# Kernel optimization log

Hardware: AMD Instinct MI355X
Metric: run time of the kernel (lower is better)

Reference implementation:

```python
import jax, jax.numpy as jnp
import numpy as np

B, NP, NC, E, C = 4, 512, 256, 128, 32
NBUCKET = 20


def soft_one_hot_linspace(x, start=0.0, end=15.0, number=NBUCKET):
    # e3nn soft_one_hot_linspace, basis='smooth_finite', cutoff=True
    values = jnp.linspace(start, end, number + 2)[1:-1]
    step = (end - start) / (number + 1)
    diff = (x[..., None] - values) / step

    def sus(y):  # exp(-1/y) for y>0 else 0 (smooth unit step)
        return jnp.where(y > 0.0, jnp.exp(-1.0 / jnp.where(y > 0.0, y, 1.0)), 0.0)

    return 1.14136 * jnp.exp(2.0) * sus(diff + 1.0) * sus(1.0 - diff)


def _init_linear(k, fan_in, fan_out):
    k1, k2 = jax.random.split(k)
    bound = 1.0 / np.sqrt(fan_in)
    W = jax.random.uniform(k1, (fan_in, fan_out), jnp.float32, -bound, bound)
    b = jax.random.uniform(k2, (fan_out,), jnp.float32, -bound, bound)
    return W, b


def setup_inputs() -> dict:
    key = jax.random.key(0)
    ks = jax.random.split(key, 12)
    inp = {}
    inp["z"] = jax.random.normal(ks[0], (B, NP, NC, E), jnp.float32)
    inp["z_mask"] = jax.random.randint(ks[1], (B, NP, NC), 0, 2) == 1
    inp["pocket_rep"] = jax.random.normal(ks[2], (B, NP, E), jnp.float32)
    inp["candidate_dis"] = jax.random.uniform(ks[3], (B, NP, NC), jnp.float32) * 16.0
    inp["W_lin"], inp["b_lin"] = _init_linear(ks[4], E, C)
    inp["W_dis"], inp["b_dis"] = _init_linear(ks[5], NBUCKET, C)
    inp["W_energy"], inp["b_energy"] = _init_linear(ks[6], C, 1)
    inp["W_gate"], inp["b_gate"] = _init_linear(ks[7], C, 1)
    inp["bias"] = jnp.ones((1,), jnp.float32)
    inp["W_energy_p"], inp["b_energy_p"] = _init_linear(ks[8], C, 1)
    inp["W_gate_p"], inp["b_gate_p"] = _init_linear(ks[9], C, 1)
    inp["bias_p"] = jnp.ones((1,), jnp.float32)
    inp["W_out"], inp["b_out"] = _init_linear(ks[10], E * C, E)
    return inp


def reference(z, z_mask, pocket_rep, candidate_dis,
              W_lin, b_lin, W_dis, b_dis,
              W_energy, b_energy, W_gate, b_gate, bias,
              W_energy_p, b_energy_p, W_gate_p, b_gate_p, bias_p,
              W_out, b_out):
    b, n_p, n_c, e = z.shape
    c = W_lin.shape[1]
    # linear + transpose(3,1): [B,Np,Nc,E] -> [B,C,Nc,Np]
    zc = jnp.transpose(z @ W_lin + b_lin, (0, 3, 2, 1))
    # softmax over last dim (Np)
    zc = jax.nn.softmax(zc, axis=-1)
    # distance-bucket bias: [B,Np,Nc,20] -> [B,Np,Nc,C] -> view [B,C,Nc,Np]
    edge_emb = soft_one_hot_linspace(candidate_dis)
    dis_bias = (edge_emb @ W_dis + b_dis).reshape(b, c, n_c, n_p)
    zc = zc + dis_bias
    # z_mask.repeat(C,1,1).view(B,C,Nc,Np) -- literal torch element order
    mask_rep = jnp.tile(z_mask, (c, 1, 1)).reshape(b, c, n_c, n_p)
    zc = jnp.where(mask_rep, jnp.asarray(1e-09, zc.dtype), zc)
    # gated energy heads on z.transpose(3,1): [B,Np,Nc,C]
    zt = jnp.transpose(zc, (0, 3, 2, 1))
    zm = z_mask.astype(zc.dtype)
    pair_energy = (jax.nn.sigmoid(zt @ W_gate + b_gate) * (zt @ W_energy + b_energy))[..., 0] * zm
    affinity_pred = jax.nn.leaky_relu(bias + pair_energy.sum(axis=(-1, -2)))
    pair_energy_p = (jax.nn.sigmoid(zt @ W_gate_p + b_gate_p) * (zt @ W_energy_p + b_energy_p))[..., 0] * zm
    prmsd_pred = jax.nn.leaky_relu(bias_p + pair_energy_p.sum(axis=(-1, -2)))
    # ligand rep: bmm([B,C*Nc,Np], [B,Np,E]) -> [B,Nc,C*E] -> Linear
    lig = jnp.einsum('bcln,bne->bcle', zc, pocket_rep)  # [B,C,Nc,E]
    lig = jnp.transpose(lig, (0, 2, 1, 3)).reshape(b, n_c, c * e)
    ligand_rep = lig @ W_out + b_out
    return (ligand_rep, affinity_pred, prmsd_pred)
```

## Files before the change

### kernel.cpp

```cpp
#include <hip/hip_runtime.h>
#include <stdint.h>


typedef float f32x4 __attribute__((ext_vector_type(4)));
typedef short s16x8 __attribute__((ext_vector_type(8)));

#define DEV static __device__ __forceinline__

DEV unsigned short f2bf(float f) {
  unsigned u = __builtin_bit_cast(unsigned, f);
  u += 0x7FFFu + ((u >> 16) & 1u);
  return (unsigned short)(u >> 16);
}
DEV float bf2f(unsigned short h) {
  unsigned u = ((unsigned)h) << 16;
  return __builtin_bit_cast(float, u);
}

__global__ void prep_k(const float* __restrict__ wlin,
                       const float* __restrict__ pocket,
                       const float* __restrict__ wout,
                       unsigned short* __restrict__ wtlin,
                       unsigned short* __restrict__ pt,
                       unsigned short* __restrict__ wto,
                       float* __restrict__ accg) {
  for (int i = blockIdx.x * 256 + threadIdx.x; i < 790536; i += gridDim.x * 256) {
    if (i < 524288) {
      int e = i >> 12, k = i & 4095;
      wto[i] = f2bf(wout[k * 128 + e]);
    } else if (i < 786432) {
      int i2 = i - 524288;
      int np = i2 & 511, r = i2 >> 9;
      int e = r & 127, b = r >> 7;
      pt[i2] = f2bf(pocket[(b * 512 + np) * 128 + e]);
    } else if (i < 790528) {
      int i3 = i - 786432;
      int k = i3 & 127, c = i3 >> 7;
      wtlin[i3] = f2bf(wlin[k * 32 + c]);
    } else {
      accg[i - 790528] = 0.0f;
    }
  }
}

extern __shared__ char smem[];

__global__ __launch_bounds__(256, 2) void mega_k(
    const float* __restrict__ z, const int* __restrict__ zmask,
    const float* __restrict__ cdis,
    const float* __restrict__ wdis, const float* __restrict__ bdis_g,
    const float* __restrict__ wE, const float* __restrict__ bE,
    const float* __restrict__ wG, const float* __restrict__ bG,
    const float* __restrict__ wEp, const float* __restrict__ bEp,
    const float* __restrict__ wGp, const float* __restrict__ bGp,
    const unsigned short* __restrict__ wtlin,
    const unsigned short* __restrict__ pt,
    unsigned short* __restrict__ lig, float* __restrict__ accg) {
  const int nc = blockIdx.x, b = blockIdx.y;
  const int t = threadIdx.x;
  const int w = t >> 6, ln = t & 63;
  const int m16 = ln & 15, q = ln >> 4;

  float* zbuf = (float*)smem;
  unsigned short* T = (unsigned short*)smem;
  unsigned short* ub = (unsigned short*)(smem + 33280);

  __shared__ float s_wd[640];
  __shared__ float s_bd[32];
  __shared__ float s_we[32], s_wg[32], s_wep[32], s_wgp[32];
  __shared__ float s_red[160];
  __shared__ float s_gmax[32], s_gsum[32];
  __shared__ unsigned long long s_mb[4][8];
  __shared__ float s_r8[8];

  if (t < 32) {
    s_bd[t] = bdis_g[t];
    s_we[t] = wE[t]; s_wg[t] = wG[t];
    s_wep[t] = wEp[t]; s_wgp[t] = wGp[t];
  }
  for (int i = t; i < 640; i += 256) s_wd[i] = wdis[i];
  for (int i = t; i < 2048; i += 256) {
    int cm = i >> 9, nn = i & 511;
    unsigned long long bal = __ballot(zmask[cm * 131072 + nc * 512 + nn] != 0);
    if ((i & 63) == 0) s_mb[cm][nn >> 6] = bal;
  }

  f32x4 acc1[8][2];
#pragma unroll
  for (int i = 0; i < 8; ++i) {
    acc1[i][0] = f32x4{0.f, 0.f, 0.f, 0.f};
    acc1[i][1] = f32x4{0.f, 0.f, 0.f, 0.f};
  }
  const int zb0 = b * 16777216 + nc * 128;
  for (int k0 = 0; k0 < 128; k0 += 32) {
    s16x8 bf0 = *(const s16x8*)(wtlin + m16 * 128 + k0 + q * 8);
    s16x8 bf1 = *(const s16x8*)(wtlin + (16 + m16) * 128 + k0 + q * 8);
    for (int h = 0; h < 2; ++h) {
      __syncthreads();
#pragma unroll
      for (int jj = 0; jj < 8; ++jj) {
        int f = jj * 256 + t;
        int row = f >> 3, qq = f & 7;
        f32x4 v = *(const f32x4*)(z + zb0 + (h * 256 + row) * 32768 + k0 + qq * 4);
        *(f32x4*)(zbuf + row * 36 + qq * 4) = v;
      }
      __syncthreads();
#pragma unroll
      for (int i = 0; i < 4; ++i) {
        int lrow = (w * 4 + i) * 16 + m16;
        f32x4 z0 = *(const f32x4*)(zbuf + lrow * 36 + q * 8);
        f32x4 z1 = *(const f32x4*)(zbuf + lrow * 36 + q * 8 + 4);
        s16x8 af;
        af[0] = (short)f2bf(z0[0]); af[1] = (short)f2bf(z0[1]);
        af[2] = (short)f2bf(z0[2]); af[3] = (short)f2bf(z0[3]);
        af[4] = (short)f2bf(z1[0]); af[5] = (short)f2bf(z1[1]);
        af[6] = (short)f2bf(z1[2]); af[7] = (short)f2bf(z1[3]);
        int ai = h * 4 + i;
        acc1[ai][0] = __builtin_amdgcn_mfma_f32_16x16x32_bf16(af, bf0, acc1[ai][0], 0, 0, 0);
        acc1[ai][1] = __builtin_amdgcn_mfma_f32_16x16x32_bf16(af, bf1, acc1[ai][1], 0, 0, 0);
      }
    }
  }

  float mx[2] = {-3.0e38f, -3.0e38f};
#pragma unroll
  for (int ai = 0; ai < 8; ++ai)
#pragma unroll
    for (int ct = 0; ct < 2; ++ct)
#pragma unroll
      for (int r = 0; r < 4; ++r) mx[ct] = fmaxf(mx[ct], acc1[ai][ct][r]);
#pragma unroll
  for (int ct = 0; ct < 2; ++ct) {
    float v = mx[ct];
    v = fmaxf(v, __shfl_xor(v, 16));
    v = fmaxf(v, __shfl_xor(v, 32));
    mx[ct] = v;
  }
  if (ln < 16) { s_red[ln * 5 + w] = mx[0]; s_red[(16 + ln) * 5 + w] = mx[1]; }
  __syncthreads();
  if (t < 32)
    s_gmax[t] = fmaxf(fmaxf(s_red[t * 5], s_red[t * 5 + 1]),
                      fmaxf(s_red[t * 5 + 2], s_red[t * 5 + 3]));
  __syncthreads();
  float sm[2] = {0.f, 0.f};
#pragma unroll
  for (int ct = 0; ct < 2; ++ct) {
    float g = s_gmax[ct * 16 + m16];
#pragma unroll
    for (int ai = 0; ai < 8; ++ai)
#pragma unroll
      for (int r = 0; r < 4; ++r) {
        float e = __expf(acc1[ai][ct][r] - g);
        acc1[ai][ct][r] = e;
        sm[ct] += e;
      }
  }
#pragma unroll
  for (int ct = 0; ct < 2; ++ct) {
    float v = sm[ct];
    v += __shfl_xor(v, 16);
    v += __shfl_xor(v, 32);
    sm[ct] = v;
  }
  if (ln < 16) { s_red[ln * 5 + w] = sm[0]; s_red[(16 + ln) * 5 + w] = sm[1]; }
  __syncthreads();
  if (t < 32)
    s_gsum[t] = 1.0f / (s_red[t * 5] + s_red[t * 5 + 1] + s_red[t * 5 + 2] + s_red[t * 5 + 3]);
  __syncthreads();

#pragma unroll
  for (int ct = 0; ct < 2; ++ct) {
    int c = ct * 16 + m16;
    float s = s_gsum[c];
#pragma unroll
    for (int ai = 0; ai < 8; ++ai) {
      int npb = (ai >> 2) * 256 + (w * 4 + (ai & 3)) * 16 + q * 4;
#pragma unroll
      for (int r = 0; r < 4; ++r) T[c * 520 + npb + r] = f2bf(acc1[ai][ct][r] * s);
    }
  }

  {
    const float SUSK = 1.14136f * __expf(2.0f);
    const int nc4 = nc >> 4, nc15 = nc & 15;
    for (int it = 0; it < 40; ++it) {
      int vid = it * 256 + t;
      int task = vid / 20, j = vid - task * 20;
      int c = task & 31, np5 = task >> 5;
      int p = 16 * c + nc4, cc = 16 * nc15 + np5;
      float d = cdis[(b * 512 + p) * 256 + cc];
      float diff = d * (21.0f / 15.0f) - (float)(j + 1);
      float y1 = diff + 1.f, y2 = 1.f - diff;
      float u = 0.f;
      if (y1 > 0.f && y2 > 0.f) u = SUSK * __expf(-1.f / y1 - 1.f / y2);
      ub[task * 24 + j] = f2bf(u);
    }
  }
  __syncthreads();

  {
    const int kg = t & 3, tg = t >> 2;
    const int cB = tg & 31, np5b = tg >> 5;
    float val[8][8];
#pragma unroll
    for (int jj = 0; jj < 8; ++jj)
#pragma unroll
      for (int kk = 0; kk < 8; ++kk) val[jj][kk] = s_bd[kg * 8 + kk];
    for (int j = 0; j < 20; ++j) {
      f32x4 wd0 = *(const f32x4*)(s_wd + j * 32 + kg * 8);
      f32x4 wd1 = *(const f32x4*)(s_wd + j * 32 + kg * 8 + 4);
#pragma unroll
      for (int jj = 0; jj < 8; ++jj) {
        float u = bf2f(ub[(tg + 64 * jj) * 24 + j]);
        val[jj][0] += u * wd0[0]; val[jj][1] += u * wd0[1];
        val[jj][2] += u * wd0[2]; val[jj][3] += u * wd0[3];
        val[jj][4] += u * wd1[0]; val[jj][5] += u * wd1[1];
        val[jj][6] += u * wd1[2]; val[jj][7] += u * wd1[3];
      }
    }
    __syncthreads();
#pragma unroll
    for (int jj = 0; jj < 8; ++jj) {
      int np5 = np5b + 2 * jj;
      int npb = np5 * 32 + kg * 8;
      unsigned short* tp = T + cB * 520 + npb;
      s16x8 tv = *(s16x8*)tp;
      unsigned long long mw = s_mb[cB & 3][npb >> 6];
      s16x8 ov;
#pragma unroll
      for (int kk = 0; kk < 8; ++kk) {
        float x = bf2f((unsigned short)tv[kk]) + val[jj][kk];
        int mk = (int)((mw >> ((npb + kk) & 63)) & 1ull);
        ov[kk] = (short)f2bf(mk ? 1e-9f : x);
      }
      *(s16x8*)tp = ov;
    }
  }
  __syncthreads();

  {
    float aff = 0.f, prm = 0.f;
    const float bg0 = bG[0], be0 = bE[0], bgp0 = bGp[0], bep0 = bEp[0];
#pragma unroll
    for (int s = 0; s < 2; ++s) {
      int np = s * 256 + t;
      float g = bg0, e = be0, gp = bgp0, ep = bep0;
      for (int c = 0; c < 32; ++c) {
        float tv = bf2f(T[c * 520 + np]);
        g += tv * s_wg[c]; e += tv * s_we[c];
        gp += tv * s_wgp[c]; ep += tv * s_wep[c];
      }
      if (zmask[(b * 512 + np) * 256 + nc] != 0) {
        aff += e / (1.f + __expf(-g));
        prm += ep / (1.f + __expf(-gp));
      }
    }
#pragma unroll
    for (int d = 32; d >= 1; d >>= 1) {
      aff += __shfl_xor(aff, d);
      prm += __shfl_xor(prm, d);
    }
    if (ln == 0) { s_r8[w] = aff; s_r8[4 + w] = prm; }
    __syncthreads();
    if (t == 0) {
      atomicAdd(accg + b, s_r8[0] + s_r8[1] + s_r8[2] + s_r8[3]);
      atomicAdd(accg + 4 + b, s_r8[4] + s_r8[5] + s_r8[6] + s_r8[7]);
    }
  }

  {
    f32x4 a5[2][2];
    a5[0][0] = f32x4{0.f, 0.f, 0.f, 0.f}; a5[0][1] = a5[0][0];
    a5[1][0] = a5[0][0]; a5[1][1] = a5[0][0];
    const unsigned short* ptb = pt + b * 65536;
    for (int k0 = 0; k0 < 512; k0 += 32) {
      s16x8 aT0 = *(const s16x8*)(T + m16 * 520 + k0 + q * 8);
      s16x8 aT1 = *(const s16x8*)(T + (16 + m16) * 520 + k0 + q * 8);
      s16x8 bP0 = *(const s16x8*)(ptb + (w * 32 + m16) * 512 + k0 + q * 8);
      s16x8 bP1 = *(const s16x8*)(ptb + (w * 32 + 16 + m16) * 512 + k0 + q * 8);
      a5[0][0] = __builtin_amdgcn_mfma_f32_16x16x32_bf16(aT0, bP0, a5[0][0], 0, 0, 0);
      a5[0][1] = __builtin_amdgcn_mfma_f32_16x16x32_bf16(aT0, bP1, a5[0][1], 0, 0, 0);
      a5[1][0] = __builtin_amdgcn_mfma_f32_16x16x32_bf16(aT1, bP0, a5[1][0], 0, 0, 0);
      a5[1][1] = __builtin_amdgcn_mfma_f32_16x16x32_bf16(aT1, bP1, a5[1][1], 0, 0, 0);
    }
    unsigned short* lg = lig + (b * 256 + nc) * 4096;
#pragma unroll
    for (int mt = 0; mt < 2; ++mt)
#pragma unroll
      for (int u = 0; u < 2; ++u)
#pragma unroll
        for (int r = 0; r < 4; ++r) {
          int c = mt * 16 + q * 4 + r;
          int e = w * 32 + u * 16 + m16;
          lg[c * 128 + e] = f2bf(a5[mt][u][r]);
        }
  }
}

__global__ __launch_bounds__(256, 2) void proj_k(
    const unsigned short* __restrict__ lig, const unsigned short* __restrict__ wto,
    float* __restrict__ part) {
  const int mb = blockIdx.x, ks = blockIdx.y;
  const int t = threadIdx.x, w = t >> 6, ln = t & 63;
  const int m16 = ln & 15, q = ln >> 4;
  f32x4 acc[2][8];
#pragma unroll
  for (int mt = 0; mt < 2; ++mt)
#pragma unroll
    for (int nt = 0; nt < 8; ++nt) acc[mt][nt] = f32x4{0.f, 0.f, 0.f, 0.f};
  const int kb = ks * 256;
  for (int k0 = 0; k0 < 256; k0 += 32) {
    s16x8 af[2], bf[8];
#pragma unroll
    for (int mt = 0; mt < 2; ++mt)
      af[mt] = *(const s16x8*)(lig + (mb * 128 + (w * 2 + mt) * 16 + m16) * 4096 + kb + k0 + q * 8);
#pragma unroll
    for (int nt = 0; nt < 8; ++nt)
      bf[nt] = *(const s16x8*)(wto + (nt * 16 + m16) * 4096 + kb + k0 + q * 8);
#pragma unroll
    for (int mt = 0; mt < 2; ++mt)
#pragma unroll
      for (int nt = 0; nt < 8; ++nt)
        acc[mt][nt] = __builtin_amdgcn_mfma_f32_16x16x32_bf16(af[mt], bf[nt], acc[mt][nt], 0, 0, 0);
  }
  float* pp = part + ks * 131072 + mb * 16384;
#pragma unroll
  for (int mt = 0; mt < 2; ++mt)
#pragma unroll
    for (int nt = 0; nt < 8; ++nt)
#pragma unroll
      for (int r = 0; r < 4; ++r)
        pp[((w * 2 + mt) * 16 + q * 4 + r) * 128 + nt * 16 + m16] = acc[mt][nt][r];
}

__global__ void reduce_k(const float* __restrict__ part, const float* __restrict__ bout,
                         const float* __restrict__ accg, const float* __restrict__ bias,
                         const float* __restrict__ biasp, float* __restrict__ out) {
  int i = blockIdx.x * 256 + threadIdx.x;
  if (i < 131072) {
    float s = bout[i & 127];
#pragma unroll
    for (int ks = 0; ks < 16; ++ks) s += part[ks * 131072 + i];
    out[i] = s;
  } else if (i < 131080) {
    int tt = i - 131072;
    float base = (tt < 4) ? bias[0] : biasp[0];
    float x = base + accg[tt];
    out[i] = (x >= 0.f) ? x : 0.01f * x;
  }
}

extern "C" void kernel_launch(void* const* d_in, const int* in_sizes, int n_in,
                              void* d_out, int out_size, void* d_ws, size_t ws_size,
                              hipStream_t stream) {
  const float* z      = (const float*)d_in[0];
  const int*   zmask  = (const int*)d_in[1];
  const float* pocket = (const float*)d_in[2];
  const float* cdis   = (const float*)d_in[3];
  const float* wlin   = (const float*)d_in[4];
  const float* wdis   = (const float*)d_in[6];
  const float* bdis   = (const float*)d_in[7];
  const float* wE     = (const float*)d_in[8];
  const float* bE     = (const float*)d_in[9];
  const float* wG     = (const float*)d_in[10];
  const float* bG     = (const float*)d_in[11];
  const float* bias   = (const float*)d_in[12];
  const float* wEp    = (const float*)d_in[13];
  const float* bEp    = (const float*)d_in[14];
  const float* wGp    = (const float*)d_in[15];
  const float* bGp    = (const float*)d_in[16];
  const float* biasp  = (const float*)d_in[17];
  const float* wout   = (const float*)d_in[18];
  const float* bout   = (const float*)d_in[19];

  char* ws = (char*)d_ws;
  float* accg           = (float*)(ws + 0);
  unsigned short* wtlin = (unsigned short*)(ws + 1024);
  unsigned short* pt    = (unsigned short*)(ws + 16384);
  unsigned short* wto   = (unsigned short*)(ws + 1048576);
  unsigned short* lig   = (unsigned short*)(ws + 2097152);
  float* part           = (float*)(ws + 10485760);
  float* outp = (float*)d_out;

  prep_k<<<1024, 256, 0, stream>>>(wlin, pocket, wout, wtlin, pt, wto, accg);
  mega_k<<<dim3(256, 4), 256, 57856, stream>>>(z, zmask, cdis, wdis, bdis,
      wE, bE, wG, bG, wEp, bEp, wGp, bGp, wtlin, pt, lig, accg);
  proj_k<<<dim3(8, 16), 256, 0, stream>>>(lig, wto, part);
  reduce_k<<<513, 256, 0, stream>>>(part, bout, accg, bias, biasp, outp);
}
```

Measured before the change: 484.3 us.

## Load z directly to registers, precompute mask bits and transposed cdis, fuse reduction via atomics

The main kernel now loads z straight from global memory into registers instead of staging it through shared memory. This cuts dynamic LDS enough to raise launch bounds to 4 blocks per CU. The prep kernel now also packs the pair mask into bitmasks, writes a transposed copy of candidate_dis, and initialises the output with b_out. The distance-bucket expansion is fused per thread, dropping the ub staging buffer and one sync. The partial-sum buffer and reduce kernel are replaced by float atomicAdd into the output, which makes summation order nondeterministic and adds atomic traffic.

```diff
diff --git a/kernel.cpp b/kernel.cpp
--- a/kernel.cpp
+++ b/kernel.cpp
@@ -20,34 +20,52 @@
 __global__ void prep_k(const float* __restrict__ wlin,
                        const float* __restrict__ pocket,
                        const float* __restrict__ wout,
+                       const int* __restrict__ zmask,
+                       const float* __restrict__ cdis,
+                       const float* __restrict__ bout,
                        unsigned short* __restrict__ wtlin,
                        unsigned short* __restrict__ pt,
                        unsigned short* __restrict__ wto,
+                       unsigned long long* __restrict__ zmb,
+                       float* __restrict__ cdisT,
+                       float* __restrict__ outp,
                        float* __restrict__ accg) {
-  for (int i = blockIdx.x * 256 + threadIdx.x; i < 790536; i += gridDim.x * 256) {
+  for (int i = blockIdx.x * 256 + threadIdx.x; i < 1970184; i += gridDim.x * 256) {
     if (i < 524288) {
-      int e = i >> 12, k = i & 4095;
-      wto[i] = f2bf(wout[k * 128 + e]);
-    } else if (i < 786432) {
-      int i2 = i - 524288;
-      int np = i2 & 511, r = i2 >> 9;
+      int np = i & 511, nc = (i >> 9) & 255, b = i >> 17;
+      unsigned long long bal = __ballot(zmask[b * 131072 + np * 256 + nc] != 0);
+      if ((i & 63) == 0) zmb[i >> 6] = bal;
+    } else if (i < 1048576) {
+      int o = i - 524288;
+      int e = o >> 12, k = o & 4095;
+      wto[o] = f2bf(wout[k * 128 + e]);
+    } else if (i < 1310720) {
+      int o = i - 1048576;
+      int np = o & 511, r = o >> 9;
       int e = r & 127, b = r >> 7;
-      pt[i2] = f2bf(pocket[(b * 512 + np) * 128 + e]);
-    } else if (i < 790528) {
-      int i3 = i - 786432;
-      int k = i3 & 127, c = i3 >> 7;
-      wtlin[i3] = f2bf(wlin[k * 32 + c]);
+      pt[o] = f2bf(pocket[(b * 512 + np) * 128 + e]);
+    } else if (i < 1314816) {
+      int o = i - 1310720;
+      int k = o & 127, c = o >> 7;
+      wtlin[o] = f2bf(wlin[k * 32 + c]);
+    } else if (i < 1314824) {
+      accg[i - 1314816] = 0.0f;
+    } else if (i < 1839112) {
+      int o = i - 1314824;
+      int c = o & 31, np5 = (o >> 5) & 15, nc = (o >> 9) & 255, b = o >> 17;
+      cdisT[o] = cdis[(b * 512 + 16 * c + (nc >> 4)) * 256 + 16 * (nc & 15) + np5];
     } else {
-      accg[i - 790528] = 0.0f;
+      int o = i - 1839112;
+      outp[o] = bout[o & 127];
     }
   }
 }
 
 extern __shared__ char smem[];
 
-__global__ __launch_bounds__(256, 2) void mega_k(
+__global__ __launch_bounds__(256, 4) void mega_k(
     const float* __restrict__ z, const int* __restrict__ zmask,
-    const float* __restrict__ cdis,
+    const float* __restrict__ cdisT,
     const float* __restrict__ wdis, const float* __restrict__ bdis_g,
     const float* __restrict__ wE, const float* __restrict__ bE,
     const float* __restrict__ wG, const float* __restrict__ bG,
@@ -55,15 +73,14 @@
     const float* __restrict__ wGp, const float* __restrict__ bGp,
     const unsigned short* __restrict__ wtlin,
     const unsigned short* __restrict__ pt,
+    const unsigned long long* __restrict__ zmb,
     unsigned short* __restrict__ lig, float* __restrict__ accg) {
   const int nc = blockIdx.x, b = blockIdx.y;
   const int t = threadIdx.x;
   const int w = t >> 6, ln = t & 63;
   const int m16 = ln & 15, q = ln >> 4;
 
-  float* zbuf = (float*)smem;
   unsigned short* T = (unsigned short*)smem;
-  unsigned short* ub = (unsigned short*)(smem + 33280);
 
   __shared__ float s_wd[640];
   __shared__ float s_bd[32];
@@ -91,31 +108,28 @@
     acc1[i][0] = f32x4{0.f, 0.f, 0.f, 0.f};
     acc1[i][1] = f32x4{0.f, 0.f, 0.f, 0.f};
   }
-  const int zb0 = b * 16777216 + nc * 128;
+  const float* zb = z + (size_t)b * 16777216 + (size_t)nc * 128;
   for (int k0 = 0; k0 < 128; k0 += 32) {
     s16x8 bf0 = *(const s16x8*)(wtlin + m16 * 128 + k0 + q * 8);
     s16x8 bf1 = *(const s16x8*)(wtlin + (16 + m16) * 128 + k0 + q * 8);
-    for (int h = 0; h < 2; ++h) {
-      __syncthreads();
-#pragma unroll
-      for (int jj = 0; jj < 8; ++jj) {
-        int f = jj * 256 + t;
-        int row = f >> 3, qq = f & 7;
-        f32x4 v = *(const f32x4*)(z + zb0 + (h * 256 + row) * 32768 + k0 + qq * 4);
-        *(f32x4*)(zbuf + row * 36 + qq * 4) = v;
-      }
-      __syncthreads();
-#pragma unroll
-      for (int i = 0; i < 4; ++i) {
-        int lrow = (w * 4 + i) * 16 + m16;
-        f32x4 z0 = *(const f32x4*)(zbuf + lrow * 36 + q * 8);
-        f32x4 z1 = *(const f32x4*)(zbuf + lrow * 36 + q * 8 + 4);
+#pragma unroll
+    for (int bt = 0; bt < 4; ++bt) {
+      f32x4 z0[2], z1[2];
+#pragma unroll
+      for (int i = 0; i < 2; ++i) {
+        int np = (w * 8 + bt * 2 + i) * 16 + m16;
+        const float* p = zb + (size_t)np * 32768 + k0 + q * 8;
+        z0[i] = *(const f32x4*)p;
+        z1[i] = *(const f32x4*)(p + 4);
+      }
+#pragma unroll
+      for (int i = 0; i < 2; ++i) {
         s16x8 af;
-        af[0] = (short)f2bf(z0[0]); af[1] = (short)f2bf(z0[1]);
-        af[2] = (short)f2bf(z0[2]); af[3] = (short)f2bf(z0[3]);
-        af[4] = (short)f2bf(z1[0]); af[5] = (short)f2bf(z1[1]);
-        af[6] = (short)f2bf(z1[2]); af[7] = (short)f2bf(z1[3]);
-        int ai = h * 4 + i;
+        af[0] = (short)f2bf(z0[i][0]); af[1] = (short)f2bf(z0[i][1]);
+        af[2] = (short)f2bf(z0[i][2]); af[3] = (short)f2bf(z0[i][3]);
+        af[4] = (short)f2bf(z1[i][0]); af[5] = (short)f2bf(z1[i][1]);
+        af[6] = (short)f2bf(z1[i][2]); af[7] = (short)f2bf(z1[i][3]);
+        int ai = bt * 2 + i;
         acc1[ai][0] = __builtin_amdgcn_mfma_f32_16x16x32_bf16(af, bf0, acc1[ai][0], 0, 0, 0);
         acc1[ai][1] = __builtin_amdgcn_mfma_f32_16x16x32_bf16(af, bf1, acc1[ai][1], 0, 0, 0);
       }
@@ -174,66 +188,50 @@
     float s = s_gsum[c];
 #pragma unroll
     for (int ai = 0; ai < 8; ++ai) {
-      int npb = (ai >> 2) * 256 + (w * 4 + (ai & 3)) * 16 + q * 4;
-#pragma unroll
-      for (int r = 0; r < 4; ++r) T[c * 520 + npb + r] = f2bf(acc1[ai][ct][r] * s);
-    }
-  }
+      int npb = (w * 8 + ai) * 16 + q * 4;
+      unsigned lo = (unsigned)f2bf(acc1[ai][ct][0] * s) |
+                    ((unsigned)f2bf(acc1[ai][ct][1] * s) << 16);
+      unsigned hi = (unsigned)f2bf(acc1[ai][ct][2] * s) |
+                    ((unsigned)f2bf(acc1[ai][ct][3] * s) << 16);
+      *(uint2*)(T + c * 520 + npb) = make_uint2(lo, hi);
+    }
+  }
+  __syncthreads();
 
   {
-    const float SUSK = 1.14136f * __expf(2.0f);
-    const int nc4 = nc >> 4, nc15 = nc & 15;
-    for (int it = 0; it < 40; ++it) {
-      int vid = it * 256 + t;
-      int task = vid / 20, j = vid - task * 20;
+    const float SUSK = 8.4335794f;
+    const float* cdb = cdisT + (size_t)(b * 256 + nc) * 512;
+#pragma unroll
+    for (int tt = 0; tt < 2; ++tt) {
+      int task = t + tt * 256;
       int c = task & 31, np5 = task >> 5;
-      int p = 16 * c + nc4, cc = 16 * nc15 + np5;
-      float d = cdis[(b * 512 + p) * 256 + cc];
-      float diff = d * (21.0f / 15.0f) - (float)(j + 1);
-      float y1 = diff + 1.f, y2 = 1.f - diff;
-      float u = 0.f;
-      if (y1 > 0.f && y2 > 0.f) u = SUSK * __expf(-1.f / y1 - 1.f / y2);
-      ub[task * 24 + j] = f2bf(u);
-    }
-  }
-  __syncthreads();
-
-  {
-    const int kg = t & 3, tg = t >> 2;
-    const int cB = tg & 31, np5b = tg >> 5;
-    float val[8][8];
-#pragma unroll
-    for (int jj = 0; jj < 8; ++jj)
-#pragma unroll
-      for (int kk = 0; kk < 8; ++kk) val[jj][kk] = s_bd[kg * 8 + kk];
-    for (int j = 0; j < 20; ++j) {
-      f32x4 wd0 = *(const f32x4*)(s_wd + j * 32 + kg * 8);
-      f32x4 wd1 = *(const f32x4*)(s_wd + j * 32 + kg * 8 + 4);
-#pragma unroll
-      for (int jj = 0; jj < 8; ++jj) {
-        float u = bf2f(ub[(tg + 64 * jj) * 24 + j]);
-        val[jj][0] += u * wd0[0]; val[jj][1] += u * wd0[1];
-        val[jj][2] += u * wd0[2]; val[jj][3] += u * wd0[3];
-        val[jj][4] += u * wd1[0]; val[jj][5] += u * wd1[1];
-        val[jj][6] += u * wd1[2]; val[jj][7] += u * wd1[3];
-      }
-    }
-    __syncthreads();
-#pragma unroll
-    for (int jj = 0; jj < 8; ++jj) {
-      int np5 = np5b + 2 * jj;
-      int npb = np5 * 32 + kg * 8;
-      unsigned short* tp = T + cB * 520 + npb;
-      s16x8 tv = *(s16x8*)tp;
-      unsigned long long mw = s_mb[cB & 3][npb >> 6];
-      s16x8 ov;
-#pragma unroll
-      for (int kk = 0; kk < 8; ++kk) {
-        float x = bf2f((unsigned short)tv[kk]) + val[jj][kk];
-        int mk = (int)((mw >> ((npb + kk) & 63)) & 1ull);
-        ov[kk] = (short)f2bf(mk ? 1e-9f : x);
-      }
-      *(s16x8*)tp = ov;
+      float d = cdb[task];
+      float val[32];
+#pragma unroll
+      for (int kk = 0; kk < 32; ++kk) val[kk] = s_bd[kk];
+      for (int j = 0; j < 20; ++j) {
+        float diff = d * (21.0f / 15.0f) - (float)(j + 1);
+        float y1 = diff + 1.f, y2 = 1.f - diff;
+        float u = 0.f;
+        if (y1 > 0.f && y2 > 0.f) u = SUSK * __expf(-1.f / y1 - 1.f / y2);
+#pragma unroll
+        for (int kk = 0; kk < 32; ++kk) val[kk] += u * s_wd[j * 32 + kk];
+      }
+      int npb = np5 * 32;
+      unsigned long long mw = s_mb[c & 3][npb >> 6];
+#pragma unroll
+      for (int kb2 = 0; kb2 < 4; ++kb2) {
+        unsigned short* tp = T + c * 520 + npb + kb2 * 8;
+        s16x8 tv = *(s16x8*)tp;
+        s16x8 ov;
+#pragma unroll
+        for (int kk = 0; kk < 8; ++kk) {
+          float x = bf2f((unsigned short)tv[kk]) + val[kb2 * 8 + kk];
+          int mk = (int)((mw >> ((npb + kb2 * 8 + kk) & 63)) & 1ull);
+          ov[kk] = (short)f2bf(mk ? 1e-9f : x);
+        }
+        *(s16x8*)tp = ov;
+      }
     }
   }
   __syncthreads();
@@ -241,6 +239,7 @@
   {
     float aff = 0.f, prm = 0.f;
     const float bg0 = bG[0], be0 = bE[0], bgp0 = bGp[0], bep0 = bEp[0];
+    const unsigned long long* zw = zmb + (size_t)(b * 256 + nc) * 8;
 #pragma unroll
     for (int s = 0; s < 2; ++s) {
       int np = s * 256 + t;
@@ -250,7 +249,7 @@
         g += tv * s_wg[c]; e += tv * s_we[c];
         gp += tv * s_wgp[c]; ep += tv * s_wep[c];
       }
-      if (zmask[(b * 512 + np) * 256 + nc] != 0) {
+      if ((zw[np >> 6] >> (np & 63)) & 1ull) {
         aff += e / (1.f + __expf(-g));
         prm += ep / (1.f + __expf(-gp));
       }
@@ -283,7 +282,7 @@
       a5[1][0] = __builtin_amdgcn_mfma_f32_16x16x32_bf16(aT1, bP0, a5[1][0], 0, 0, 0);
       a5[1][1] = __builtin_amdgcn_mfma_f32_16x16x32_bf16(aT1, bP1, a5[1][1], 0, 0, 0);
     }
-    unsigned short* lg = lig + (b * 256 + nc) * 4096;
+    unsigned short* lg = lig + (size_t)(b * 256 + nc) * 4096;
 #pragma unroll
     for (int mt = 0; mt < 2; ++mt)
 #pragma unroll
@@ -299,7 +298,8 @@
 
 __global__ __launch_bounds__(256, 2) void proj_k(
     const unsigned short* __restrict__ lig, const unsigned short* __restrict__ wto,
-    float* __restrict__ part) {
+    const float* __restrict__ accg, const float* __restrict__ bias,
+    const float* __restrict__ biasp, float* __restrict__ outp) {
   const int mb = blockIdx.x, ks = blockIdx.y;
   const int t = threadIdx.x, w = t >> 6, ln = t & 63;
   const int m16 = ln & 15, q = ln >> 4;
@@ -313,40 +313,28 @@
     s16x8 af[2], bf[8];
 #pragma unroll
     for (int mt = 0; mt < 2; ++mt)
-      af[mt] = *(const s16x8*)(lig + (mb * 128 + (w * 2 + mt) * 16 + m16) * 4096 + kb + k0 + q * 8);
+      af[mt] = *(const s16x8*)(lig + (size_t)(mb * 128 + (w * 2 + mt) * 16 + m16) * 4096 + kb + k0 + q * 8);
 #pragma unroll
     for (int nt = 0; nt < 8; ++nt)
-      bf[nt] = *(const s16x8*)(wto + (nt * 16 + m16) * 4096 + kb + k0 + q * 8);
+      bf[nt] = *(const s16x8*)(wto + (size_t)(nt * 16 + m16) * 4096 + kb + k0 + q * 8);
 #pragma unroll
     for (int mt = 0; mt < 2; ++mt)
 #pragma unroll
       for (int nt = 0; nt < 8; ++nt)
         acc[mt][nt] = __builtin_amdgcn_mfma_f32_16x16x32_bf16(af[mt], bf[nt], acc[mt][nt], 0, 0, 0);
   }
-  float* pp = part + ks * 131072 + mb * 16384;
 #pragma unroll
   for (int mt = 0; mt < 2; ++mt)
 #pragma unroll
     for (int nt = 0; nt < 8; ++nt)
 #pragma unroll
       for (int r = 0; r < 4; ++r)
-        pp[((w * 2 + mt) * 16 + q * 4 + r) * 128 + nt * 16 + m16] = acc[mt][nt][r];
-}
-
-__global__ void reduce_k(const float* __restrict__ part, const float* __restrict__ bout,
-                         const float* __restrict__ accg, const float* __restrict__ bias,
-                         const float* __restrict__ biasp, float* __restrict__ out) {
-  int i = blockIdx.x * 256 + threadIdx.x;
-  if (i < 131072) {
-    float s = bout[i & 127];
-#pragma unroll
-    for (int ks = 0; ks < 16; ++ks) s += part[ks * 131072 + i];
-    out[i] = s;
-  } else if (i < 131080) {
-    int tt = i - 131072;
-    float base = (tt < 4) ? bias[0] : biasp[0];
-    float x = base + accg[tt];
-    out[i] = (x >= 0.f) ? x : 0.01f * x;
+        atomicAdd(outp + (size_t)(mb * 128 + (w * 2 + mt) * 16 + q * 4 + r) * 128 + nt * 16 + m16,
+                  acc[mt][nt][r]);
+  if (mb == 0 && ks == 0 && t < 8) {
+    float base = (t < 4) ? bias[0] : biasp[0];
+    float x = base + accg[t];
+    outp[131072 + t] = (x >= 0.f) ? x : 0.01f * x;
   }
 }
 
@@ -374,17 +362,18 @@
   const float* bout   = (const float*)d_in[19];
 
   char* ws = (char*)d_ws;
-  float* accg           = (float*)(ws + 0);
-  unsigned short* wtlin = (unsigned short*)(ws + 1024);
-  unsigned short* pt    = (unsigned short*)(ws + 16384);
-  unsigned short* wto   = (unsigned short*)(ws + 1048576);
-  unsigned short* lig   = (unsigned short*)(ws + 2097152);
-  float* part           = (float*)(ws + 10485760);
+  float* accg                  = (float*)(ws + 0);
+  unsigned short* wtlin        = (unsigned short*)(ws + 1024);
+  unsigned long long* zmb      = (unsigned long long*)(ws + 16384);
+  unsigned short* pt           = (unsigned short*)(ws + 131072);
+  float* cdisT                 = (float*)(ws + 655360);
+  unsigned short* wto          = (unsigned short*)(ws + 2752512);
+  unsigned short* lig          = (unsigned short*)(ws + 4194304);
   float* outp = (float*)d_out;
 
-  prep_k<<<1024, 256, 0, stream>>>(wlin, pocket, wout, wtlin, pt, wto, accg);
-  mega_k<<<dim3(256, 4), 256, 57856, stream>>>(z, zmask, cdis, wdis, bdis,
-      wE, bE, wG, bG, wEp, bEp, wGp, bGp, wtlin, pt, lig, accg);
-  proj_k<<<dim3(8, 16), 256, 0, stream>>>(lig, wto, part);
-  reduce_k<<<513, 256, 0, stream>>>(part, bout, accg, bias, biasp, outp);
-}
+  prep_k<<<1024, 256, 0, stream>>>(wlin, pocket, wout, zmask, cdis, bout,
+                                   wtlin, pt, wto, zmb, cdisT, outp, accg);
+  mega_k<<<dim3(256, 4), 256, 33280, stream>>>(z, zmask, cdisT, wdis, bdis,
+      wE, bE, wG, bG, wEp, bEp, wGp, bGp, wtlin, pt, zmb, lig, accg);
+  proj_k<<<dim3(8, 16), 256, 0, stream>>>(lig, wto, accg, bias, biasp, outp);
+}
```

New measurement: 471.0 us. 2.7% less time.
